# Kernel optimization log

Measured on AMD Instinct MI355X. Metric: run time of the kernel, lower is better.

Reference implementation:

```python
import jax, jax.numpy as jnp
import numpy as np

TEMPERATURE = 0.07
BASE_TEMPERATURE = 0.07


def _pairwise_euclid(x):
    # torch.cdist(x, x, p=2), with safe sqrt (zero grad at zero distance)
    sq = jnp.sum(x * x, axis=1)
    d2 = sq[:, None] + sq[None, :] - 2.0 * (x @ x.T)
    d2 = jnp.maximum(d2, 0.0)
    safe = jnp.where(d2 > 0.0, d2, 1.0)
    return jnp.where(d2 > 0.0, jnp.sqrt(safe), 0.0)


def setup_inputs() -> dict:
    key = jax.random.key(0)
    k1, k2 = jax.random.split(key)
    features = jax.random.normal(k1, (1024, 2, 512), dtype=jnp.float32)
    labels = jax.random.uniform(k2, (1024,), dtype=jnp.float32)
    return {"features": features, "labels": labels}


def reference(features, labels):
    B, V, D = features.shape
    N = B * V
    # torch.cat(torch.unbind(features, dim=1), dim=0): views stacked -> [N, D]
    cf = features.transpose(1, 0, 2).reshape(N, D)
    lab = jnp.tile(labels, V)  # label of row i is labels[i % B]

    dist = _pairwise_euclid(cf)              # [N, N]
    logits = -dist / TEMPERATURE
    eye = jnp.eye(N, dtype=logits.dtype)
    w = jnp.exp(logits) * (1.0 - eye)        # exp(logits) with l == i excluded

    dis = jnp.abs(lab[:, None] - lab[None, :])  # |y_i - y_j|, symmetric

    # negative[i, j] = sum_{l != i, |y_l - y_i| >= |y_i - y_j|} exp(logits[i, l])
    # computed per-row via sort + suffix cumsum + searchsorted (O(N^2 log N))
    order = jnp.argsort(dis, axis=1)
    sorted_d = jnp.take_along_axis(dis, order, axis=1)
    sorted_w = jnp.take_along_axis(w, order, axis=1)
    suffix = jnp.flip(jnp.cumsum(jnp.flip(sorted_w, axis=1), axis=1), axis=1)
    suffix = jnp.concatenate([suffix, jnp.zeros((N, 1), suffix.dtype)], axis=1)  # [N, N+1]
    # side='left': counts entries strictly < d, so suffix[idx] sums all >= d (ties incl.)
    idx = jax.vmap(lambda sd, d: jnp.searchsorted(sd, d, side='left'))(sorted_d, dis)
    negative = jnp.take_along_axis(suffix, idx, axis=1)
    negative = negative * (1.0 - eye) + eye  # diag set to 1 (log -> 0)

    logits_z = logits * (1.0 - eye)          # logits[i, i] = 0
    log_prob = logits_z - jnp.log(negative)
    mean_log_prob_pos = jnp.sum(log_prob, axis=1) / (N - 1)
    loss = -(TEMPERATURE / BASE_TEMPERATURE) * jnp.mean(mean_log_prob_pos)
    return loss
```

## Files before the change

kernel.cpp:

```cpp
#include <hip/hip_runtime.h>
#include <math.h>


#define NN 2048
#define BB 1024
#define DD 512
#define NT 256
#define NEGINF (-INFINITY)
#define CS 64.0f

typedef short s16x8 __attribute__((ext_vector_type(8)));
typedef float f32x4 __attribute__((ext_vector_type(4)));

__device__ __forceinline__ const float* cf_row(const float* F, int i) {
    return F + ((size_t)(i & (BB - 1)) * 2 + (size_t)(i >> 10)) * DD;
}

__device__ __forceinline__ unsigned bf_rne(float x) {
    const unsigned u = __float_as_uint(x);
    return (u + 0x7FFFu + ((u >> 16) & 1u)) >> 16;
}
__device__ __forceinline__ float bf_val(unsigned h) {
    return __uint_as_float(h << 16);
}

__global__ __launch_bounds__(512) void sort_labels_kernel(const float* __restrict__ labels,
                                                          float* __restrict__ slab,
                                                          int* __restrict__ sj) {
    __shared__ float kk[BB];
    __shared__ int   id[BB];
    const int t = threadIdx.x;
    #pragma unroll
    for (int e = 0; e < 2; ++e) { const int p = t + e * 512; kk[p] = labels[p]; id[p] = p; }
    for (int k = 2; k <= BB; k <<= 1) {
        for (int j = k >> 1; j > 0; j >>= 1) {
            if (j >= 32) __syncthreads();
            else __builtin_amdgcn_wave_barrier();
            #pragma unroll
            for (int e = 0; e < 2; ++e) {
                const int idx = t + e * 512;
                const int ixj = idx ^ j;
                if (ixj > idx) {
                    const float k1 = kk[idx], k2 = kk[ixj];
                    const bool up = ((idx & k) == 0);
                    if (up ? (k1 > k2) : (k1 < k2)) {
                        kk[idx] = k2; kk[ixj] = k1;
                        const int i1 = id[idx]; id[idx] = id[ixj]; id[ixj] = i1;
                    }
                }
            }
        }
    }
    __syncthreads();
    #pragma unroll
    for (int e = 0; e < 2; ++e) {
        const int p = t + e * 512;
        const float lv = kk[p];
        const int b = id[p];
        slab[2 * p] = lv; slab[2 * p + 1] = lv;
        sj[2 * p] = b;    sj[2 * p + 1] = b + BB;
    }
}

__global__ __launch_bounds__(256) void prep_split_kernel(const float* __restrict__ F,
                                                         ushort* __restrict__ Ahi,
                                                         ushort* __restrict__ Alo,
                                                         float* __restrict__ sq) {
    const int t = threadIdx.x;
    const int lane = t & 63;
    const int w = t >> 6;
    const int i = blockIdx.x * 4 + w;
    const float* src = cf_row(F, i);
    const float4 v0 = reinterpret_cast<const float4*>(src)[lane];
    const float4 v1 = reinterpret_cast<const float4*>(src)[lane + 64];
    float ss = v0.x * v0.x + v0.y * v0.y + v0.z * v0.z + v0.w * v0.w
             + v1.x * v1.x + v1.y * v1.y + v1.z * v1.z + v1.w * v1.w;
    #pragma unroll
    for (int st = 32; st > 0; st >>= 1) ss += __shfl_down(ss, st);
    if (lane == 0) sq[i] = ss;

    const float a[8] = {v0.x, v0.y, v0.z, v0.w, v1.x, v1.y, v1.z, v1.w};
    ushort h[8], l[8];
    #pragma unroll
    for (int e = 0; e < 8; ++e) {
        const unsigned hb = bf_rne(a[e]);
        h[e] = (ushort)hb;
        l[e] = (ushort)bf_rne(a[e] - bf_val(hb));
    }
    const size_t base = (size_t)i * DD;
    *reinterpret_cast<ushort4*>(&Ahi[base + lane * 4])       = make_ushort4(h[0], h[1], h[2], h[3]);
    *reinterpret_cast<ushort4*>(&Ahi[base + 256 + lane * 4]) = make_ushort4(h[4], h[5], h[6], h[7]);
    *reinterpret_cast<ushort4*>(&Alo[base + lane * 4])       = make_ushort4(l[0], l[1], l[2], l[3]);
    *reinterpret_cast<ushort4*>(&Alo[base + 256 + lane * 4]) = make_ushort4(l[4], l[5], l[6], l[7]);
}

#define TM 128
#define TN 64
#define TK 32
__global__ __launch_bounds__(256) void gemm_dist_kernel(const ushort* __restrict__ Ahi,
                                                        const ushort* __restrict__ Alo,
                                                        const float* __restrict__ sq,
                                                        const int* __restrict__ sj,
                                                        float* __restrict__ distp) {
    __shared__ ushort Ah[4][TM][8];
    __shared__ ushort Al[4][TM][8];
    __shared__ ushort Bh[4][TN][8];
    __shared__ ushort Bl[4][TN][8];
    __shared__ int   sjcA[TM];
    __shared__ int   sjcB[TN];
    __shared__ float sqA[TM];
    __shared__ float sqB[TN];

    const int t = threadIdx.x;
    const int lane = t & 63;
    const int w = t >> 6;

    const int id = blockIdx.x;
    int by = (int)((__fsqrt_rn(4.0f * (float)id + 1.0f) - 1.0f) * 0.5f);
    while ((by + 1) * (by + 2) <= id) ++by;
    while (by * (by + 1) > id) --by;
    const int bx = id - by * (by + 1);
    const int row0 = by * TM;
    const int col0 = bx * TN;
    const bool below = (bx < 2 * by);

    if (t < TM) {
        const int s = sj[row0 + t];
        sjcA[t] = s; sqA[t] = sq[s];
    } else if (t < TM + TN) {
        const int u = t - TM;
        const int s = sj[col0 + u];
        sjcB[u] = s; sqB[u] = sq[s];
    }
    __syncthreads();
    const int rr = t >> 2;
    const int cq = t & 3;
    const size_t gA0 = (size_t)sjcA[rr] * DD + cq * 8;
    const size_t gA1 = (size_t)sjcA[64 + rr] * DD + cq * 8;
    const size_t gB0 = (size_t)sjcB[rr] * DD + cq * 8;

    f32x4 acc[2][4] = {};
    const int m = lane & 15;
    const int q = lane >> 4;

    for (int kt = 0; kt < DD / TK; ++kt) {
        __syncthreads();
        const size_t ko = (size_t)kt * TK;
        *reinterpret_cast<int4*>(&Ah[cq][rr][0])      = *reinterpret_cast<const int4*>(&Ahi[gA0 + ko]);
        *reinterpret_cast<int4*>(&Al[cq][rr][0])      = *reinterpret_cast<const int4*>(&Alo[gA0 + ko]);
        *reinterpret_cast<int4*>(&Ah[cq][64 + rr][0]) = *reinterpret_cast<const int4*>(&Ahi[gA1 + ko]);
        *reinterpret_cast<int4*>(&Al[cq][64 + rr][0]) = *reinterpret_cast<const int4*>(&Alo[gA1 + ko]);
        *reinterpret_cast<int4*>(&Bh[cq][rr][0])      = *reinterpret_cast<const int4*>(&Ahi[gB0 + ko]);
        *reinterpret_cast<int4*>(&Bl[cq][rr][0])      = *reinterpret_cast<const int4*>(&Alo[gB0 + ko]);
        __syncthreads();

        s16x8 fah[2], fal[2], fbh[4], fbl[4];
        #pragma unroll
        for (int mt = 0; mt < 2; ++mt) {
            fah[mt] = *reinterpret_cast<const s16x8*>(&Ah[q][w * 32 + mt * 16 + m][0]);
            fal[mt] = *reinterpret_cast<const s16x8*>(&Al[q][w * 32 + mt * 16 + m][0]);
        }
        #pragma unroll
        for (int nt = 0; nt < 4; ++nt) {
            fbh[nt] = *reinterpret_cast<const s16x8*>(&Bh[q][nt * 16 + m][0]);
            fbl[nt] = *reinterpret_cast<const s16x8*>(&Bl[q][nt * 16 + m][0]);
        }
        #pragma unroll
        for (int mt = 0; mt < 2; ++mt)
            #pragma unroll
            for (int nt = 0; nt < 4; ++nt) {
                acc[mt][nt] = __builtin_amdgcn_mfma_f32_16x16x32_bf16(fah[mt], fbh[nt], acc[mt][nt], 0, 0, 0);
                acc[mt][nt] = __builtin_amdgcn_mfma_f32_16x16x32_bf16(fah[mt], fbl[nt], acc[mt][nt], 0, 0, 0);
                acc[mt][nt] = __builtin_amdgcn_mfma_f32_16x16x32_bf16(fal[mt], fbh[nt], acc[mt][nt], 0, 0, 0);
            }
    }

    #pragma unroll
    for (int mt = 0; mt < 2; ++mt) {
        const int lr0 = w * 32 + mt * 16 + q * 4;
        #pragma unroll
        for (int nt = 0; nt < 4; ++nt) {
            const int lc = nt * 16 + m;
            float o[4];
            #pragma unroll
            for (int r = 0; r < 4; ++r) {
                const float d2 = sqA[lr0 + r] + sqB[lc] - 2.0f * acc[mt][nt][r];
                o[r] = (d2 > 0.f) ? sqrtf(d2) : 0.f;
            }
            #pragma unroll
            for (int r = 0; r < 4; ++r)
                distp[(size_t)(row0 + lr0 + r) * NN + col0 + lc] = o[r];
            if (below) {
                const float4 o4 = make_float4(o[0], o[1], o[2], o[3]);
                *reinterpret_cast<float4*>(&distp[(size_t)(col0 + lc) * NN + row0 + lr0]) = o4;
            }
        }
    }
}

__device__ __forceinline__ int bs_right(const float* key, float d, int lo, int hi) {
    while (lo < hi) {
        const int mid = (lo + hi) >> 1;
        if (key[mid] >= d) hi = mid; else lo = mid + 1;
    }
    return lo;
}
__device__ __forceinline__ int bs_left(const float* key, float d, int lo, int hi) {
    while (lo < hi) {
        const int mid = (lo + hi) >> 1;
        if (key[mid] < d) hi = mid; else lo = mid + 1;
    }
    return lo;
}

__global__ __launch_bounds__(256) void row_kernel(const float* __restrict__ distp,
                                                  const float* __restrict__ slab,
                                                  double* __restrict__ rowval) {
    __shared__ float key[NN];
    __shared__ float Pf[NN];
    __shared__ float Sf[NN + 1];
    __shared__ float wmxA[4], wmxB[4], wps[4], wss[4];
    __shared__ double wDA[4], wLA[4], wDB[4], wLB[4];

    const int pr = blockIdx.x;
    const int rA = 2 * pr, rB = 2 * pr + 1;
    const int t = threadIdx.x;
    const int lane = t & 63;
    const int w = t >> 6;
    const float x = slab[rA];
    const float negInvT = -1.0f / 0.07f;
    const float* drowA = &distp[(size_t)rA * NN];
    const float* drowB = &distp[(size_t)rB * NN];

    #pragma unroll
    for (int e = 0; e < 2; ++e) {
        const int p4 = t + e * NT;
        const float4 l4 = reinterpret_cast<const float4*>(slab)[p4];
        key[p4 * 4 + 0] = fabsf(l4.x - x);
        key[p4 * 4 + 1] = fabsf(l4.y - x);
        key[p4 * 4 + 2] = fabsf(l4.z - x);
        key[p4 * 4 + 3] = fabsf(l4.w - x);
    }
    const int cb = t * 8;
    float vA[8], vB[8];
    double dsumA = 0.0, dsumB = 0.0;
    float mxA = NEGINF, mxB = NEGINF;
    #pragma unroll
    for (int e = 0; e < 2; ++e) {
        const float4 a4 = reinterpret_cast<const float4*>(drowA)[2 * t + e];
        const float4 b4 = reinterpret_cast<const float4*>(drowB)[2 * t + e];
        const float av[4] = {a4.x, a4.y, a4.z, a4.w};
        const float bv[4] = {b4.x, b4.y, b4.z, b4.w};
        #pragma unroll
        for (int c = 0; c < 4; ++c) {
            const int pc = cb + e * 4 + c;
            if (pc == rA) vA[e * 4 + c] = NEGINF;
            else { const float vv = av[c] * negInvT; vA[e * 4 + c] = vv; mxA = fmaxf(mxA, vv); dsumA += (double)av[c]; }
            if (pc == rB) vB[e * 4 + c] = NEGINF;
            else { const float vv = bv[c] * negInvT; vB[e * 4 + c] = vv; mxB = fmaxf(mxB, vv); dsumB += (double)bv[c]; }
        }
    }
    #pragma unroll
    for (int st = 32; st > 0; st >>= 1) {
        mxA = fmaxf(mxA, __shfl_down(mxA, st));
        mxB = fmaxf(mxB, __shfl_down(mxB, st));
    }
    if (lane == 0) { wmxA[w] = mxA; wmxB[w] = mxB; }
    __syncthreads();
    const float MA = fmaxf(fmaxf(wmxA[0], wmxA[1]), fmaxf(wmxA[2], wmxA[3]));
    const float MB = fmaxf(fmaxf(wmxB[0], wmxB[1]), fmaxf(wmxB[2], wmxB[3]));

    int L8[8], R8[8];
    const int a = cb, b = cb + 7;
    {
        const int le = (rA - 1 < b) ? rA - 1 : b;
        if (a <= le) {
            const float da = key[a];
            const int Ra = bs_right(key, da, rA, NN);
            int Rl = Ra;
            if (le > a) Rl = bs_right(key, key[le], rA, Ra);
            for (int p = a; p <= le; ++p) {
                const float d = key[p];
                int R;
                if (p == a) R = Ra;
                else if (p == le) R = Rl;
                else R = bs_right(key, d, Rl, Ra);
                int L = p + 1;
                while (L < rA && key[L] == d) ++L;
                L8[p - a] = L; R8[p - a] = R;
            }
        }
        const int rs = (rA + 1 > a) ? rA + 1 : a;
        if (rs <= b) {
            const float dr = key[rs];
            const int Lr = bs_left(key, dr, 0, rA);
            int Lb = Lr;
            if (b > rs) Lb = bs_left(key, key[b], 0, Lr);
            for (int p = rs; p <= b; ++p) {
                const float d = key[p];
                int L;
                if (p == rs) L = Lr;
                else if (p == b) L = Lb;
                else L = bs_left(key, d, Lb, Lr);
                int R = p;
                while (R > rA && key[R - 1] == d) --R;
                L8[p - a] = L; R8[p - a] = R;
            }
        }
        if (rA >= a && rA <= b) { L8[rA - a] = rA; R8[rA - a] = rA; }
    }

    double lnsumA = 0.0;
    {
        float e8[8];
        #pragma unroll
        for (int jj = 0; jj < 8; ++jj) e8[jj] = __expf(vA[jj] - MA + CS);
        {
            float run = 0.f, ex[8];
            #pragma unroll
            for (int jj = 0; jj < 8; ++jj) { ex[jj] = run; run += e8[jj]; }
            float inc = run;
            #pragma unroll
            for (int st = 1; st < 64; st <<= 1) {
                const float nm = __shfl_up(inc, st);
                if (lane >= st) inc += nm;
            }
            float xofs = __shfl_up(inc, 1);
            if (lane == 0) xofs = 0.f;
            if (lane == 63) wps[w] = inc;
            __syncthreads();
            #pragma unroll
            for (int ww = 0; ww < 3; ++ww)
                if (ww < w) xofs += wps[ww];
            #pragma unroll
            for (int jj = 0; jj < 8; ++jj) Pf[cb + jj] = ex[jj] + xofs;
        }
        {
            float run = 0.f, sx[8];
            #pragma unroll
            for (int jj = 7; jj >= 0; --jj) { run += e8[jj]; sx[jj] = run; }
            float inc = run;
            #pragma unroll
            for (int st = 1; st < 64; st <<= 1) {
                const float nm = __shfl_down(inc, st);
                if (lane + st < 64) inc += nm;
            }
            float xofs = __shfl_down(inc, 1);
            if (lane == 63) xofs = 0.f;
            if (lane == 0) wss[w] = inc;
            __syncthreads();
            #pragma unroll
            for (int ww = 1; ww < 4; ++ww)
                if (ww > w) xofs += wss[ww];
            #pragma unroll
            for (int jj = 0; jj < 8; ++jj) Sf[cb + jj] = sx[jj] + xofs;
            if (t == 0) Sf[NN] = 0.f;
        }
        __syncthreads();
        const float MBA = MA - CS;
        #pragma unroll
        for (int jj = 0; jj < 8; ++jj) {
            const int p = cb + jj;
            if (p == rA) continue;
            const float s = fmaxf(Pf[L8[jj]] + Sf[R8[jj]], 1e-38f);
            lnsumA += (double)(MBA + __logf(s));
        }
    }
    __syncthreads();

    double lnsumB = 0.0;
    {
        float e8[8];
        #pragma unroll
        for (int jj = 0; jj < 8; ++jj) e8[jj] = __expf(vB[jj] - MB + CS);
        {
            float run = 0.f, ex[8];
            #pragma unroll
            for (int jj = 0; jj < 8; ++jj) { ex[jj] = run; run += e8[jj]; }
            float inc = run;
            #pragma unroll
            for (int st = 1; st < 64; st <<= 1) {
                const float nm = __shfl_up(inc, st);
                if (lane >= st) inc += nm;
            }
            float xofs = __shfl_up(inc, 1);
            if (lane == 0) xofs = 0.f;
            if (lane == 63) wps[w] = inc;
            __syncthreads();
            #pragma unroll
            for (int ww = 0; ww < 3; ++ww)
                if (ww < w) xofs += wps[ww];
            #pragma unroll
            for (int jj = 0; jj < 8; ++jj) Pf[cb + jj] = ex[jj] + xofs;
        }
        {
            float run = 0.f, sx[8];
            #pragma unroll
            for (int jj = 7; jj >= 0; --jj) { run += e8[jj]; sx[jj] = run; }
            float inc = run;
            #pragma unroll
            for (int st = 1; st < 64; st <<= 1) {
                const float nm = __shfl_down(inc, st);
                if (lane + st < 64) inc += nm;
            }
            float xofs = __shfl_down(inc, 1);
            if (lane == 63) xofs = 0.f;
            if (lane == 0) wss[w] = inc;
            __syncthreads();
            #pragma unroll
            for (int ww = 1; ww < 4; ++ww)
                if (ww > w) xofs += wss[ww];
            #pragma unroll
            for (int jj = 0; jj < 8; ++jj) Sf[cb + jj] = sx[jj] + xofs;
            if (t == 0) Sf[NN] = 0.f;
        }
        __syncthreads();
        const float MBB = MB - CS;
        #pragma unroll
        for (int jj = 0; jj < 8; ++jj) {
            const int p = cb + jj;
            if (p == rB) continue;
            const float s = fmaxf(Pf[L8[jj]] + Sf[R8[jj]], 1e-38f);
            lnsumB += (double)(MBB + __logf(s));
        }
    }

    #pragma unroll
    for (int st = 32; st > 0; st >>= 1) {
        dsumA  += __shfl_down(dsumA, st);
        lnsumA += __shfl_down(lnsumA, st);
        dsumB  += __shfl_down(dsumB, st);
        lnsumB += __shfl_down(lnsumB, st);
    }
    if (lane == 0) { wDA[w] = dsumA; wLA[w] = lnsumA; wDB[w] = dsumB; wLB[w] = lnsumB; }
    __syncthreads();
    if (t == 0) {
        rowval[rA] = (-(wDA[0] + wDA[1] + wDA[2] + wDA[3]) / 0.07)
                   - (wLA[0] + wLA[1] + wLA[2] + wLA[3]);
        rowval[rB] = (-(wDB[0] + wDB[1] + wDB[2] + wDB[3]) / 0.07)
                   - (wLB[0] + wLB[1] + wLB[2] + wLB[3]);
    }
}

__global__ __launch_bounds__(256) void finalize_kernel(const double* __restrict__ rowval,
                                                       float* __restrict__ out) {
    __shared__ double red[NT];
    const int t = threadIdx.x;
    double s = 0.0;
    for (int j = t; j < NN; j += NT) s += rowval[j];
    red[t] = s;
    __syncthreads();
    for (int ofs = NT / 2; ofs > 0; ofs >>= 1) {
        if (t < ofs) red[t] += red[t + ofs];
        __syncthreads();
    }
    if (t == 0) {
        out[0] = (float)(-red[0] / ((double)NN * (double)(NN - 1)));
    }
}

extern "C" void kernel_launch(void* const* d_in, const int* in_sizes, int n_in,
                              void* d_out, int out_size, void* d_ws, size_t ws_size,
                              hipStream_t stream) {
    const float* features = (const float*)d_in[0];
    const float* labels   = (const float*)d_in[1];
    float* out = (float*)d_out;

    char* ws = (char*)d_ws;
    size_t off = 0;
    float*  sq     = (float*) (ws + off); off += NN * sizeof(float);
    float*  slab   = (float*) (ws + off); off += NN * sizeof(float);
    int*    sj     = (int*)   (ws + off); off += NN * sizeof(int);
    double* rowval = (double*)(ws + off); off += NN * sizeof(double);
    ushort* Ahi    = (ushort*)(ws + off); off += (size_t)NN * DD * sizeof(ushort);
    ushort* Alo    = (ushort*)(ws + off); off += (size_t)NN * DD * sizeof(ushort);
    float*  distp  = (float*) (ws + off); off += (size_t)NN * NN * sizeof(float);

    sort_labels_kernel<<<1, 512, 0, stream>>>(labels, slab, sj);
    prep_split_kernel<<<NN / 4, NT, 0, stream>>>(features, Ahi, Alo, sq);
    gemm_dist_kernel<<<16 * 17, NT, 0, stream>>>(Ahi, Alo, sq, sj, distp);
    row_kernel<<<NN / 2, NT, 0, stream>>>(distp, slab, rowval);
    finalize_kernel<<<1, NT, 0, stream>>>(rowval, out);
}
```

Baseline: 133.1 us.

## Fuse label ranking sort into prep kernel, shrink GEMM tiles, widen row blocks

Replaces the single-block bitonic label sort with a parallel rank-counting sort placed in extra blocks of the feature split/prep kernel, removing one launch and the serial sort latency. Halves the GEMM row tile to 64 so the triangular grid has more blocks to fill the GPU, at the cost of less operand reuse per block. Row kernel uses 512 threads with 4 elements per thread for more parallelism per row pair.

```diff
diff --git a/kernel.cpp b/kernel.cpp
--- a/kernel.cpp
+++ b/kernel.cpp
@@ -24,77 +24,68 @@
     return __uint_as_float(h << 16);
 }
 
-__global__ __launch_bounds__(512) void sort_labels_kernel(const float* __restrict__ labels,
-                                                          float* __restrict__ slab,
-                                                          int* __restrict__ sj) {
-    __shared__ float kk[BB];
-    __shared__ int   id[BB];
+__global__ __launch_bounds__(512) void prep_sort_kernel(const float* __restrict__ F,
+                                                        const float* __restrict__ labels,
+                                                        ushort* __restrict__ Ahi,
+                                                        ushort* __restrict__ Alo,
+                                                        float* __restrict__ sq,
+                                                        float* __restrict__ slab,
+                                                        int* __restrict__ sj) {
+    __shared__ float lab[BB];
+    const int blk = blockIdx.x;
     const int t = threadIdx.x;
-    #pragma unroll
-    for (int e = 0; e < 2; ++e) { const int p = t + e * 512; kk[p] = labels[p]; id[p] = p; }
-    for (int k = 2; k <= BB; k <<= 1) {
-        for (int j = k >> 1; j > 0; j >>= 1) {
-            if (j >= 32) __syncthreads();
-            else __builtin_amdgcn_wave_barrier();
-            #pragma unroll
-            for (int e = 0; e < 2; ++e) {
-                const int idx = t + e * 512;
-                const int ixj = idx ^ j;
-                if (ixj > idx) {
-                    const float k1 = kk[idx], k2 = kk[ixj];
-                    const bool up = ((idx & k) == 0);
-                    if (up ? (k1 > k2) : (k1 < k2)) {
-                        kk[idx] = k2; kk[ixj] = k1;
-                        const int i1 = id[idx]; id[idx] = id[ixj]; id[ixj] = i1;
-                    }
-                }
-            }
-        }
-    }
-    __syncthreads();
-    #pragma unroll
-    for (int e = 0; e < 2; ++e) {
-        const int p = t + e * 512;
-        const float lv = kk[p];
-        const int b = id[p];
-        slab[2 * p] = lv; slab[2 * p + 1] = lv;
-        sj[2 * p] = b;    sj[2 * p + 1] = b + BB;
-    }
-}
-
-__global__ __launch_bounds__(256) void prep_split_kernel(const float* __restrict__ F,
-                                                         ushort* __restrict__ Ahi,
-                                                         ushort* __restrict__ Alo,
-                                                         float* __restrict__ sq) {
-    const int t = threadIdx.x;
-    const int lane = t & 63;
-    const int w = t >> 6;
-    const int i = blockIdx.x * 4 + w;
-    const float* src = cf_row(F, i);
-    const float4 v0 = reinterpret_cast<const float4*>(src)[lane];
-    const float4 v1 = reinterpret_cast<const float4*>(src)[lane + 64];
-    float ss = v0.x * v0.x + v0.y * v0.y + v0.z * v0.z + v0.w * v0.w
-             + v1.x * v1.x + v1.y * v1.y + v1.z * v1.z + v1.w * v1.w;
-    #pragma unroll
-    for (int st = 32; st > 0; st >>= 1) ss += __shfl_down(ss, st);
-    if (lane == 0) sq[i] = ss;
-
-    const float a[8] = {v0.x, v0.y, v0.z, v0.w, v1.x, v1.y, v1.z, v1.w};
-    ushort h[8], l[8];
-    #pragma unroll
-    for (int e = 0; e < 8; ++e) {
-        const unsigned hb = bf_rne(a[e]);
-        h[e] = (ushort)hb;
-        l[e] = (ushort)bf_rne(a[e] - bf_val(hb));
-    }
-    const size_t base = (size_t)i * DD;
-    *reinterpret_cast<ushort4*>(&Ahi[base + lane * 4])       = make_ushort4(h[0], h[1], h[2], h[3]);
-    *reinterpret_cast<ushort4*>(&Ahi[base + 256 + lane * 4]) = make_ushort4(h[4], h[5], h[6], h[7]);
-    *reinterpret_cast<ushort4*>(&Alo[base + lane * 4])       = make_ushort4(l[0], l[1], l[2], l[3]);
-    *reinterpret_cast<ushort4*>(&Alo[base + 256 + lane * 4]) = make_ushort4(l[4], l[5], l[6], l[7]);
-}
-
-#define TM 128
+
+    if (blk < 256) {
+        const int lane = t & 63;
+        const int w = t >> 6;
+        const int i = blk * 8 + w;
+        const float* src = cf_row(F, i);
+        const float4 v0 = reinterpret_cast<const float4*>(src)[lane];
+        const float4 v1 = reinterpret_cast<const float4*>(src)[lane + 64];
+        float ss = v0.x * v0.x + v0.y * v0.y + v0.z * v0.z + v0.w * v0.w
+                 + v1.x * v1.x + v1.y * v1.y + v1.z * v1.z + v1.w * v1.w;
+        #pragma unroll
+        for (int st = 32; st > 0; st >>= 1) ss += __shfl_down(ss, st);
+        if (lane == 0) sq[i] = ss;
+
+        const float a[8] = {v0.x, v0.y, v0.z, v0.w, v1.x, v1.y, v1.z, v1.w};
+        ushort h[8], l[8];
+        #pragma unroll
+        for (int e = 0; e < 8; ++e) {
+            const unsigned hb = bf_rne(a[e]);
+            h[e] = (ushort)hb;
+            l[e] = (ushort)bf_rne(a[e] - bf_val(hb));
+        }
+        const size_t base = (size_t)i * DD;
+        *reinterpret_cast<ushort4*>(&Ahi[base + lane * 4])       = make_ushort4(h[0], h[1], h[2], h[3]);
+        *reinterpret_cast<ushort4*>(&Ahi[base + 256 + lane * 4]) = make_ushort4(h[4], h[5], h[6], h[7]);
+        *reinterpret_cast<ushort4*>(&Alo[base + lane * 4])       = make_ushort4(l[0], l[1], l[2], l[3]);
+        *reinterpret_cast<ushort4*>(&Alo[base + 256 + lane * 4]) = make_ushort4(l[4], l[5], l[6], l[7]);
+    } else {
+        lab[t] = labels[t];
+        lab[t + 512] = labels[t + 512];
+        __syncthreads();
+        const int e = (blk - 256) * 512 + t;
+        const float li = lab[e];
+        int rank = 0;
+        const float4* l4 = reinterpret_cast<const float4*>(lab);
+        #pragma unroll 4
+        for (int j = 0; j < BB / 4; ++j) {
+            const float4 v = l4[j];
+            const int j0 = j * 4;
+            rank += (v.x < li) || (v.x == li && (j0 + 0) < e);
+            rank += (v.y < li) || (v.y == li && (j0 + 1) < e);
+            rank += (v.z < li) || (v.z == li && (j0 + 2) < e);
+            rank += (v.w < li) || (v.w == li && (j0 + 3) < e);
+        }
+        slab[2 * rank]     = li;
+        slab[2 * rank + 1] = li;
+        sj[2 * rank]     = e;
+        sj[2 * rank + 1] = e + BB;
+    }
+}
+
+#define TM 64
 #define TN 64
 #define TK 32
 __global__ __launch_bounds__(256) void gemm_dist_kernel(const ushort* __restrict__ Ahi,
@@ -116,13 +107,13 @@
     const int w = t >> 6;
 
     const int id = blockIdx.x;
-    int by = (int)((__fsqrt_rn(4.0f * (float)id + 1.0f) - 1.0f) * 0.5f);
-    while ((by + 1) * (by + 2) <= id) ++by;
-    while (by * (by + 1) > id) --by;
-    const int bx = id - by * (by + 1);
+    int by = (int)((__fsqrt_rn(8.0f * (float)id + 1.0f) - 1.0f) * 0.5f);
+    while ((by + 1) * (by + 2) / 2 <= id) ++by;
+    while (by * (by + 1) / 2 > id) --by;
+    const int bx = id - by * (by + 1) / 2;
     const int row0 = by * TM;
     const int col0 = bx * TN;
-    const bool below = (bx < 2 * by);
+    const bool below = (bx < by);
 
     if (t < TM) {
         const int s = sj[row0 + t];
@@ -135,65 +126,50 @@
     __syncthreads();
     const int rr = t >> 2;
     const int cq = t & 3;
-    const size_t gA0 = (size_t)sjcA[rr] * DD + cq * 8;
-    const size_t gA1 = (size_t)sjcA[64 + rr] * DD + cq * 8;
-    const size_t gB0 = (size_t)sjcB[rr] * DD + cq * 8;
-
-    f32x4 acc[2][4] = {};
+    const size_t gA = (size_t)sjcA[rr] * DD + cq * 8;
+    const size_t gB = (size_t)sjcB[rr] * DD + cq * 8;
+
+    f32x4 acc[4] = {};
     const int m = lane & 15;
     const int q = lane >> 4;
 
     for (int kt = 0; kt < DD / TK; ++kt) {
         __syncthreads();
         const size_t ko = (size_t)kt * TK;
-        *reinterpret_cast<int4*>(&Ah[cq][rr][0])      = *reinterpret_cast<const int4*>(&Ahi[gA0 + ko]);
-        *reinterpret_cast<int4*>(&Al[cq][rr][0])      = *reinterpret_cast<const int4*>(&Alo[gA0 + ko]);
-        *reinterpret_cast<int4*>(&Ah[cq][64 + rr][0]) = *reinterpret_cast<const int4*>(&Ahi[gA1 + ko]);
-        *reinterpret_cast<int4*>(&Al[cq][64 + rr][0]) = *reinterpret_cast<const int4*>(&Alo[gA1 + ko]);
-        *reinterpret_cast<int4*>(&Bh[cq][rr][0])      = *reinterpret_cast<const int4*>(&Ahi[gB0 + ko]);
-        *reinterpret_cast<int4*>(&Bl[cq][rr][0])      = *reinterpret_cast<const int4*>(&Alo[gB0 + ko]);
-        __syncthreads();
-
-        s16x8 fah[2], fal[2], fbh[4], fbl[4];
-        #pragma unroll
-        for (int mt = 0; mt < 2; ++mt) {
-            fah[mt] = *reinterpret_cast<const s16x8*>(&Ah[q][w * 32 + mt * 16 + m][0]);
-            fal[mt] = *reinterpret_cast<const s16x8*>(&Al[q][w * 32 + mt * 16 + m][0]);
-        }
+        *reinterpret_cast<int4*>(&Ah[cq][rr][0]) = *reinterpret_cast<const int4*>(&Ahi[gA + ko]);
+        *reinterpret_cast<int4*>(&Al[cq][rr][0]) = *reinterpret_cast<const int4*>(&Alo[gA + ko]);
+        *reinterpret_cast<int4*>(&Bh[cq][rr][0]) = *reinterpret_cast<const int4*>(&Ahi[gB + ko]);
+        *reinterpret_cast<int4*>(&Bl[cq][rr][0]) = *reinterpret_cast<const int4*>(&Alo[gB + ko]);
+        __syncthreads();
+
+        const s16x8 fah = *reinterpret_cast<const s16x8*>(&Ah[q][w * 16 + m][0]);
+        const s16x8 fal = *reinterpret_cast<const s16x8*>(&Al[q][w * 16 + m][0]);
         #pragma unroll
         for (int nt = 0; nt < 4; ++nt) {
-            fbh[nt] = *reinterpret_cast<const s16x8*>(&Bh[q][nt * 16 + m][0]);
-            fbl[nt] = *reinterpret_cast<const s16x8*>(&Bl[q][nt * 16 + m][0]);
-        }
-        #pragma unroll
-        for (int mt = 0; mt < 2; ++mt)
-            #pragma unroll
-            for (int nt = 0; nt < 4; ++nt) {
-                acc[mt][nt] = __builtin_amdgcn_mfma_f32_16x16x32_bf16(fah[mt], fbh[nt], acc[mt][nt], 0, 0, 0);
-                acc[mt][nt] = __builtin_amdgcn_mfma_f32_16x16x32_bf16(fah[mt], fbl[nt], acc[mt][nt], 0, 0, 0);
-                acc[mt][nt] = __builtin_amdgcn_mfma_f32_16x16x32_bf16(fal[mt], fbh[nt], acc[mt][nt], 0, 0, 0);
-            }
-    }
-
+            const s16x8 fbh = *reinterpret_cast<const s16x8*>(&Bh[q][nt * 16 + m][0]);
+            const s16x8 fbl = *reinterpret_cast<const s16x8*>(&Bl[q][nt * 16 + m][0]);
+            acc[nt] = __builtin_amdgcn_mfma_f32_16x16x32_bf16(fah, fbh, acc[nt], 0, 0, 0);
+            acc[nt] = __builtin_amdgcn_mfma_f32_16x16x32_bf16(fah, fbl, acc[nt], 0, 0, 0);
+            acc[nt] = __builtin_amdgcn_mfma_f32_16x16x32_bf16(fal, fbh, acc[nt], 0, 0, 0);
+        }
+    }
+
+    const int lr0 = w * 16 + q * 4;
     #pragma unroll
-    for (int mt = 0; mt < 2; ++mt) {
-        const int lr0 = w * 32 + mt * 16 + q * 4;
-        #pragma unroll
-        for (int nt = 0; nt < 4; ++nt) {
-            const int lc = nt * 16 + m;
-            float o[4];
-            #pragma unroll
-            for (int r = 0; r < 4; ++r) {
-                const float d2 = sqA[lr0 + r] + sqB[lc] - 2.0f * acc[mt][nt][r];
-                o[r] = (d2 > 0.f) ? sqrtf(d2) : 0.f;
-            }
-            #pragma unroll
-            for (int r = 0; r < 4; ++r)
-                distp[(size_t)(row0 + lr0 + r) * NN + col0 + lc] = o[r];
-            if (below) {
-                const float4 o4 = make_float4(o[0], o[1], o[2], o[3]);
-                *reinterpret_cast<float4*>(&distp[(size_t)(col0 + lc) * NN + row0 + lr0]) = o4;
-            }
+    for (int nt = 0; nt < 4; ++nt) {
+        const int lc = nt * 16 + m;
+        float o[4];
+        #pragma unroll
+        for (int r = 0; r < 4; ++r) {
+            const float d2 = sqA[lr0 + r] + sqB[lc] - 2.0f * acc[nt][r];
+            o[r] = (d2 > 0.f) ? sqrtf(d2) : 0.f;
+        }
+        #pragma unroll
+        for (int r = 0; r < 4; ++r)
+            distp[(size_t)(row0 + lr0 + r) * NN + col0 + lc] = o[r];
+        if (below) {
+            const float4 o4 = make_float4(o[0], o[1], o[2], o[3]);
+            *reinterpret_cast<float4*>(&distp[(size_t)(col0 + lc) * NN + row0 + lr0]) = o4;
         }
     }
 }
@@ -213,14 +189,14 @@
     return lo;
 }
 
-__global__ __launch_bounds__(256) void row_kernel(const float* __restrict__ distp,
+__global__ __launch_bounds__(512) void row_kernel(const float* __restrict__ distp,
                                                   const float* __restrict__ slab,
                                                   double* __restrict__ rowval) {
     __shared__ float key[NN];
     __shared__ float Pf[NN];
     __shared__ float Sf[NN + 1];
-    __shared__ float wmxA[4], wmxB[4], wps[4], wss[4];
-    __shared__ double wDA[4], wLA[4], wDB[4], wLB[4];
+    __shared__ float wmxA[8], wmxB[8], wps[8], wss[8];
+    __shared__ double wDA[8], wLA[8], wDB[8], wLB[8];
 
     const int pr = blockIdx.x;
     const int rA = 2 * pr, rB = 2 * pr + 1;
@@ -232,32 +208,29 @@
     const float* drowA = &distp[(size_t)rA * NN];
     const float* drowB = &distp[(size_t)rB * NN];
 
-    #pragma unroll
-    for (int e = 0; e < 2; ++e) {
-        const int p4 = t + e * NT;
-        const float4 l4 = reinterpret_cast<const float4*>(slab)[p4];
-        key[p4 * 4 + 0] = fabsf(l4.x - x);
-        key[p4 * 4 + 1] = fabsf(l4.y - x);
-        key[p4 * 4 + 2] = fabsf(l4.z - x);
-        key[p4 * 4 + 3] = fabsf(l4.w - x);
-    }
-    const int cb = t * 8;
-    float vA[8], vB[8];
+    {
+        const float4 l4 = reinterpret_cast<const float4*>(slab)[t];
+        key[t * 4 + 0] = fabsf(l4.x - x);
+        key[t * 4 + 1] = fabsf(l4.y - x);
+        key[t * 4 + 2] = fabsf(l4.z - x);
+        key[t * 4 + 3] = fabsf(l4.w - x);
+    }
+    const int cb = t * 4;
+    float vA[4], vB[4];
     double dsumA = 0.0, dsumB = 0.0;
     float mxA = NEGINF, mxB = NEGINF;
-    #pragma unroll
-    for (int e = 0; e < 2; ++e) {
-        const float4 a4 = reinterpret_cast<const float4*>(drowA)[2 * t + e];
-        const float4 b4 = reinterpret_cast<const float4*>(drowB)[2 * t + e];
+    {
+        const float4 a4 = reinterpret_cast<const float4*>(drowA)[t];
+        const float4 b4 = reinterpret_cast<const float4*>(drowB)[t];
         const float av[4] = {a4.x, a4.y, a4.z, a4.w};
         const float bv[4] = {b4.x, b4.y, b4.z, b4.w};
         #pragma unroll
         for (int c = 0; c < 4; ++c) {
-            const int pc = cb + e * 4 + c;
-            if (pc == rA) vA[e * 4 + c] = NEGINF;
-            else { const float vv = av[c] * negInvT; vA[e * 4 + c] = vv; mxA = fmaxf(mxA, vv); dsumA += (double)av[c]; }
-            if (pc == rB) vB[e * 4 + c] = NEGINF;
-            else { const float vv = bv[c] * negInvT; vB[e * 4 + c] = vv; mxB = fmaxf(mxB, vv); dsumB += (double)bv[c]; }
+            const int pc = cb + c;
+            if (pc == rA) vA[c] = NEGINF;
+            else { const float vv = av[c] * negInvT; vA[c] = vv; mxA = fmaxf(mxA, vv); dsumA += (double)av[c]; }
+            if (pc == rB) vB[c] = NEGINF;
+            else { const float vv = bv[c] * negInvT; vB[c] = vv; mxB = fmaxf(mxB, vv); dsumB += (double)bv[c]; }
         }
     }
     #pragma unroll
@@ -267,11 +240,13 @@
     }
     if (lane == 0) { wmxA[w] = mxA; wmxB[w] = mxB; }
     __syncthreads();
-    const float MA = fmaxf(fmaxf(wmxA[0], wmxA[1]), fmaxf(wmxA[2], wmxA[3]));
-    const float MB = fmaxf(fmaxf(wmxB[0], wmxB[1]), fmaxf(wmxB[2], wmxB[3]));
-
-    int L8[8], R8[8];
-    const int a = cb, b = cb + 7;
+    const float MA = fmaxf(fmaxf(fmaxf(wmxA[0], wmxA[1]), fmaxf(wmxA[2], wmxA[3])),
+                           fmaxf(fmaxf(wmxA[4], wmxA[5]), fmaxf(wmxA[6], wmxA[7])));
+    const float MB = fmaxf(fmaxf(fmaxf(wmxB[0], wmxB[1]), fmaxf(wmxB[2], wmxB[3])),
+                           fmaxf(fmaxf(wmxB[4], wmxB[5]), fmaxf(wmxB[6], wmxB[7])));
+
+    int L8[4], R8[4];
+    const int a = cb, b = cb + 3;
     {
         const int le = (rA - 1 < b) ? rA - 1 : b;
         if (a <= le) {
@@ -312,13 +287,13 @@
 
     double lnsumA = 0.0;
     {
-        float e8[8];
-        #pragma unroll
-        for (int jj = 0; jj < 8; ++jj) e8[jj] = __expf(vA[jj] - MA + CS);
+        float e8[4];
+        #pragma unroll
+        for (int jj = 0; jj < 4; ++jj) e8[jj] = __expf(vA[jj] - MA + CS);
         {
-            float run = 0.f, ex[8];
-            #pragma unroll
-            for (int jj = 0; jj < 8; ++jj) { ex[jj] = run; run += e8[jj]; }
+            float run = 0.f, ex[4];
+            #pragma unroll
+            for (int jj = 0; jj < 4; ++jj) { ex[jj] = run; run += e8[jj]; }
             float inc = run;
             #pragma unroll
             for (int st = 1; st < 64; st <<= 1) {
@@ -330,15 +305,15 @@
             if (lane == 63) wps[w] = inc;
             __syncthreads();
             #pragma unroll
-            for (int ww = 0; ww < 3; ++ww)
+            for (int ww = 0; ww < 7; ++ww)
                 if (ww < w) xofs += wps[ww];
             #pragma unroll
-            for (int jj = 0; jj < 8; ++jj) Pf[cb + jj] = ex[jj] + xofs;
+            for (int jj = 0; jj < 4; ++jj) Pf[cb + jj] = ex[jj] + xofs;
         }
         {
-            float run = 0.f, sx[8];
-            #pragma unroll
-            for (int jj = 7; jj >= 0; --jj) { run += e8[jj]; sx[jj] = run; }
+            float run = 0.f, sx[4];
+            #pragma unroll
+            for (int jj = 3; jj >= 0; --jj) { run += e8[jj]; sx[jj] = run; }
             float inc = run;
             #pragma unroll
             for (int st = 1; st < 64; st <<= 1) {
@@ -350,16 +325,16 @@
             if (lane == 0) wss[w] = inc;
             __syncthreads();
             #pragma unroll
-            for (int ww = 1; ww < 4; ++ww)
+            for (int ww = 1; ww < 8; ++ww)
                 if (ww > w) xofs += wss[ww];
             #pragma unroll
-            for (int jj = 0; jj < 8; ++jj) Sf[cb + jj] = sx[jj] + xofs;
+            for (int jj = 0; jj < 4; ++jj) Sf[cb + jj] = sx[jj] + xofs;
             if (t == 0) Sf[NN] = 0.f;
         }
         __syncthreads();
         const float MBA = MA - CS;
         #pragma unroll
-        for (int jj = 0; jj < 8; ++jj) {
+        for (int jj = 0; jj < 4; ++jj) {
             const int p = cb + jj;
             if (p == rA) continue;
             const float s = fmaxf(Pf[L8[jj]] + Sf[R8[jj]], 1e-38f);
@@ -370,13 +345,13 @@
 
     double lnsumB = 0.0;
     {
-        float e8[8];
-        #pragma unroll
-        for (int jj = 0; jj < 8; ++jj) e8[jj] = __expf(vB[jj] - MB + CS);
+        float e8[4];
+        #pragma unroll
+        for (int jj = 0; jj < 4; ++jj) e8[jj] = __expf(vB[jj] - MB + CS);
         {
-            float run = 0.f, ex[8];
-            #pragma unroll
-            for (int jj = 0; jj < 8; ++jj) { ex[jj] = run; run += e8[jj]; }
+            float run = 0.f, ex[4];
+            #pragma unroll
+            for (int jj = 0; jj < 4; ++jj) { ex[jj] = run; run += e8[jj]; }
             float inc = run;
             #pragma unroll
             for (int st = 1; st < 64; st <<= 1) {
@@ -388,15 +363,15 @@
             if (lane == 63) wps[w] = inc;
             __syncthreads();
             #pragma unroll
-            for (int ww = 0; ww < 3; ++ww)
+            for (int ww = 0; ww < 7; ++ww)
                 if (ww < w) xofs += wps[ww];
             #pragma unroll
-            for (int jj = 0; jj < 8; ++jj) Pf[cb + jj] = ex[jj] + xofs;
+            for (int jj = 0; jj < 4; ++jj) Pf[cb + jj] = ex[jj] + xofs;
         }
         {
-            float run = 0.f, sx[8];
-            #pragma unroll
-            for (int jj = 7; jj >= 0; --jj) { run += e8[jj]; sx[jj] = run; }
+            float run = 0.f, sx[4];
+            #pragma unroll
+            for (int jj = 3; jj >= 0; --jj) { run += e8[jj]; sx[jj] = run; }
             float inc = run;
             #pragma unroll
             for (int st = 1; st < 64; st <<= 1) {
@@ -408,16 +383,16 @@
             if (lane == 0) wss[w] = inc;
             __syncthreads();
             #pragma unroll
-            for (int ww = 1; ww < 4; ++ww)
+            for (int ww = 1; ww < 8; ++ww)
                 if (ww > w) xofs += wss[ww];
             #pragma unroll
-            for (int jj = 0; jj < 8; ++jj) Sf[cb + jj] = sx[jj] + xofs;
+            for (int jj = 0; jj < 4; ++jj) Sf[cb + jj] = sx[jj] + xofs;
             if (t == 0) Sf[NN] = 0.f;
         }
         __syncthreads();
         const float MBB = MB - CS;
         #pragma unroll
-        for (int jj = 0; jj < 8; ++jj) {
+        for (int jj = 0; jj < 4; ++jj) {
             const int p = cb + jj;
             if (p == rB) continue;
             const float s = fmaxf(Pf[L8[jj]] + Sf[R8[jj]], 1e-38f);
@@ -435,10 +410,11 @@
     if (lane == 0) { wDA[w] = dsumA; wLA[w] = lnsumA; wDB[w] = dsumB; wLB[w] = lnsumB; }
     __syncthreads();
     if (t == 0) {
-        rowval[rA] = (-(wDA[0] + wDA[1] + wDA[2] + wDA[3]) / 0.07)
-                   - (wLA[0] + wLA[1] + wLA[2] + wLA[3]);
-        rowval[rB] = (-(wDB[0] + wDB[1] + wDB[2] + wDB[3]) / 0.07)
-                   - (wLB[0] + wLB[1] + wLB[2] + wLB[3]);
+        double dA = 0.0, lA = 0.0, dB = 0.0, lB = 0.0;
+        #pragma unroll
+        for (int ww = 0; ww < 8; ++ww) { dA += wDA[ww]; lA += wLA[ww]; dB += wDB[ww]; lB += wLB[ww]; }
+        rowval[rA] = (-dA / 0.07) - lA;
+        rowval[rB] = (-dB / 0.07) - lB;
     }
 }
 
@@ -476,9 +452,8 @@
     ushort* Alo    = (ushort*)(ws + off); off += (size_t)NN * DD * sizeof(ushort);
     float*  distp  = (float*) (ws + off); off += (size_t)NN * NN * sizeof(float);
 
-    sort_labels_kernel<<<1, 512, 0, stream>>>(labels, slab, sj);
-    prep_split_kernel<<<NN / 4, NT, 0, stream>>>(features, Ahi, Alo, sq);
-    gemm_dist_kernel<<<16 * 17, NT, 0, stream>>>(Ahi, Alo, sq, sj, distp);
-    row_kernel<<<NN / 2, NT, 0, stream>>>(distp, slab, rowval);
+    prep_sort_kernel<<<258, 512, 0, stream>>>(features, labels, Ahi, Alo, sq, slab, sj);
+    gemm_dist_kernel<<<528, NT, 0, stream>>>(Ahi, Alo, sq, sj, distp);
+    row_kernel<<<NN / 2, 512, 0, stream>>>(distp, slab, rowval);
     finalize_kernel<<<1, NT, 0, stream>>>(rowval, out);
 }
```

Measured after the change: 136.7 us. 2.7% more time.

## Fuse label sort into prep kernel via rank sort; fold finalize into row kernel

Applied to the files above, without the earlier changes.

Replaces the single-block bitonic label sort with a parallel rank-counting sort, run as two extra blocks inside the feature split/prep kernel, so the sort and the bf16 split happen in one launch. The separate finalize kernel is removed: each row-pair block atomically adds its double contribution, and the last block (found with an atomic counter) writes the loss. This cuts two kernel launches and the serial bitonic stage. The cost is global atomics and a summation order that is no longer deterministic. The rank sort does O(N) compares per element.

```diff
diff --git a/kernel.cpp b/kernel.cpp
--- a/kernel.cpp
+++ b/kernel.cpp
@@ -24,74 +24,68 @@
     return __uint_as_float(h << 16);
 }
 
-__global__ __launch_bounds__(512) void sort_labels_kernel(const float* __restrict__ labels,
-                                                          float* __restrict__ slab,
-                                                          int* __restrict__ sj) {
-    __shared__ float kk[BB];
-    __shared__ int   id[BB];
+__global__ __launch_bounds__(512) void prep_sort_kernel(const float* __restrict__ F,
+                                                        const float* __restrict__ labels,
+                                                        ushort* __restrict__ Ahi,
+                                                        ushort* __restrict__ Alo,
+                                                        float* __restrict__ sq,
+                                                        float* __restrict__ slab,
+                                                        int* __restrict__ sj,
+                                                        double* __restrict__ accd,
+                                                        int* __restrict__ cnt) {
+    __shared__ float lab[BB];
+    const int blk = blockIdx.x;
     const int t = threadIdx.x;
-    #pragma unroll
-    for (int e = 0; e < 2; ++e) { const int p = t + e * 512; kk[p] = labels[p]; id[p] = p; }
-    for (int k = 2; k <= BB; k <<= 1) {
-        for (int j = k >> 1; j > 0; j >>= 1) {
-            if (j >= 32) __syncthreads();
-            else __builtin_amdgcn_wave_barrier();
-            #pragma unroll
-            for (int e = 0; e < 2; ++e) {
-                const int idx = t + e * 512;
-                const int ixj = idx ^ j;
-                if (ixj > idx) {
-                    const float k1 = kk[idx], k2 = kk[ixj];
-                    const bool up = ((idx & k) == 0);
-                    if (up ? (k1 > k2) : (k1 < k2)) {
-                        kk[idx] = k2; kk[ixj] = k1;
-                        const int i1 = id[idx]; id[idx] = id[ixj]; id[ixj] = i1;
-                    }
-                }
-            }
-        }
-    }
-    __syncthreads();
-    #pragma unroll
-    for (int e = 0; e < 2; ++e) {
-        const int p = t + e * 512;
-        const float lv = kk[p];
-        const int b = id[p];
-        slab[2 * p] = lv; slab[2 * p + 1] = lv;
-        sj[2 * p] = b;    sj[2 * p + 1] = b + BB;
-    }
-}
-
-__global__ __launch_bounds__(256) void prep_split_kernel(const float* __restrict__ F,
-                                                         ushort* __restrict__ Ahi,
-                                                         ushort* __restrict__ Alo,
-                                                         float* __restrict__ sq) {
-    const int t = threadIdx.x;
-    const int lane = t & 63;
-    const int w = t >> 6;
-    const int i = blockIdx.x * 4 + w;
-    const float* src = cf_row(F, i);
-    const float4 v0 = reinterpret_cast<const float4*>(src)[lane];
-    const float4 v1 = reinterpret_cast<const float4*>(src)[lane + 64];
-    float ss = v0.x * v0.x + v0.y * v0.y + v0.z * v0.z + v0.w * v0.w
-             + v1.x * v1.x + v1.y * v1.y + v1.z * v1.z + v1.w * v1.w;
-    #pragma unroll
-    for (int st = 32; st > 0; st >>= 1) ss += __shfl_down(ss, st);
-    if (lane == 0) sq[i] = ss;
-
-    const float a[8] = {v0.x, v0.y, v0.z, v0.w, v1.x, v1.y, v1.z, v1.w};
-    ushort h[8], l[8];
-    #pragma unroll
-    for (int e = 0; e < 8; ++e) {
-        const unsigned hb = bf_rne(a[e]);
-        h[e] = (ushort)hb;
-        l[e] = (ushort)bf_rne(a[e] - bf_val(hb));
-    }
-    const size_t base = (size_t)i * DD;
-    *reinterpret_cast<ushort4*>(&Ahi[base + lane * 4])       = make_ushort4(h[0], h[1], h[2], h[3]);
-    *reinterpret_cast<ushort4*>(&Ahi[base + 256 + lane * 4]) = make_ushort4(h[4], h[5], h[6], h[7]);
-    *reinterpret_cast<ushort4*>(&Alo[base + lane * 4])       = make_ushort4(l[0], l[1], l[2], l[3]);
-    *reinterpret_cast<ushort4*>(&Alo[base + 256 + lane * 4]) = make_ushort4(l[4], l[5], l[6], l[7]);
+
+    if (blk < 256) {
+        const int lane = t & 63;
+        const int w = t >> 6;
+        const int i = blk * 8 + w;
+        const float* src = cf_row(F, i);
+        const float4 v0 = reinterpret_cast<const float4*>(src)[lane];
+        const float4 v1 = reinterpret_cast<const float4*>(src)[lane + 64];
+        float ss = v0.x * v0.x + v0.y * v0.y + v0.z * v0.z + v0.w * v0.w
+                 + v1.x * v1.x + v1.y * v1.y + v1.z * v1.z + v1.w * v1.w;
+        #pragma unroll
+        for (int st = 32; st > 0; st >>= 1) ss += __shfl_down(ss, st);
+        if (lane == 0) sq[i] = ss;
+
+        const float a[8] = {v0.x, v0.y, v0.z, v0.w, v1.x, v1.y, v1.z, v1.w};
+        ushort h[8], l[8];
+        #pragma unroll
+        for (int e = 0; e < 8; ++e) {
+            const unsigned hb = bf_rne(a[e]);
+            h[e] = (ushort)hb;
+            l[e] = (ushort)bf_rne(a[e] - bf_val(hb));
+        }
+        const size_t base = (size_t)i * DD;
+        *reinterpret_cast<ushort4*>(&Ahi[base + lane * 4])       = make_ushort4(h[0], h[1], h[2], h[3]);
+        *reinterpret_cast<ushort4*>(&Ahi[base + 256 + lane * 4]) = make_ushort4(h[4], h[5], h[6], h[7]);
+        *reinterpret_cast<ushort4*>(&Alo[base + lane * 4])       = make_ushort4(l[0], l[1], l[2], l[3]);
+        *reinterpret_cast<ushort4*>(&Alo[base + 256 + lane * 4]) = make_ushort4(l[4], l[5], l[6], l[7]);
+    } else {
+        if (blk == 257 && t == 0) { *accd = 0.0; *cnt = 0; }
+        lab[t] = labels[t];
+        lab[t + 512] = labels[t + 512];
+        __syncthreads();
+        const int e = (blk - 256) * 512 + t;
+        const float li = lab[e];
+        int rank = 0;
+        const float4* l4 = reinterpret_cast<const float4*>(lab);
+        #pragma unroll 4
+        for (int j = 0; j < BB / 4; ++j) {
+            const float4 v = l4[j];
+            const int j0 = j * 4;
+            rank += (v.x < li) || (v.x == li && (j0 + 0) < e);
+            rank += (v.y < li) || (v.y == li && (j0 + 1) < e);
+            rank += (v.z < li) || (v.z == li && (j0 + 2) < e);
+            rank += (v.w < li) || (v.w == li && (j0 + 3) < e);
+        }
+        slab[2 * rank]     = li;
+        slab[2 * rank + 1] = li;
+        sj[2 * rank]     = e;
+        sj[2 * rank + 1] = e + BB;
+    }
 }
 
 #define TM 128
@@ -215,7 +209,9 @@
 
 __global__ __launch_bounds__(256) void row_kernel(const float* __restrict__ distp,
                                                   const float* __restrict__ slab,
-                                                  double* __restrict__ rowval) {
+                                                  double* __restrict__ accd,
+                                                  int* __restrict__ cnt,
+                                                  float* __restrict__ out) {
     __shared__ float key[NN];
     __shared__ float Pf[NN];
     __shared__ float Sf[NN + 1];
@@ -435,27 +431,18 @@
     if (lane == 0) { wDA[w] = dsumA; wLA[w] = lnsumA; wDB[w] = dsumB; wLB[w] = lnsumB; }
     __syncthreads();
     if (t == 0) {
-        rowval[rA] = (-(wDA[0] + wDA[1] + wDA[2] + wDA[3]) / 0.07)
-                   - (wLA[0] + wLA[1] + wLA[2] + wLA[3]);
-        rowval[rB] = (-(wDB[0] + wDB[1] + wDB[2] + wDB[3]) / 0.07)
-                   - (wLB[0] + wLB[1] + wLB[2] + wLB[3]);
-    }
-}
-
-__global__ __launch_bounds__(256) void finalize_kernel(const double* __restrict__ rowval,
-                                                       float* __restrict__ out) {
-    __shared__ double red[NT];
-    const int t = threadIdx.x;
-    double s = 0.0;
-    for (int j = t; j < NN; j += NT) s += rowval[j];
-    red[t] = s;
-    __syncthreads();
-    for (int ofs = NT / 2; ofs > 0; ofs >>= 1) {
-        if (t < ofs) red[t] += red[t + ofs];
-        __syncthreads();
-    }
-    if (t == 0) {
-        out[0] = (float)(-red[0] / ((double)NN * (double)(NN - 1)));
+        const double pairv = ((-(wDA[0] + wDA[1] + wDA[2] + wDA[3]) / 0.07)
+                              - (wLA[0] + wLA[1] + wLA[2] + wLA[3]))
+                           + ((-(wDB[0] + wDB[1] + wDB[2] + wDB[3]) / 0.07)
+                              - (wLB[0] + wLB[1] + wLB[2] + wLB[3]));
+        atomicAdd(accd, pairv);
+        __threadfence();
+        const int old = atomicAdd(cnt, 1);
+        if (old == NN / 2 - 1) {
+            __threadfence();
+            const double tot = atomicAdd(accd, 0.0);
+            out[0] = (float)(-tot / ((double)NN * (double)(NN - 1)));
+        }
     }
 }
 
@@ -471,14 +458,13 @@
     float*  sq     = (float*) (ws + off); off += NN * sizeof(float);
     float*  slab   = (float*) (ws + off); off += NN * sizeof(float);
     int*    sj     = (int*)   (ws + off); off += NN * sizeof(int);
-    double* rowval = (double*)(ws + off); off += NN * sizeof(double);
+    double* accd   = (double*)(ws + off); off += sizeof(double);
+    int*    cnt    = (int*)   (ws + off); off += 2 * sizeof(int);
     ushort* Ahi    = (ushort*)(ws + off); off += (size_t)NN * DD * sizeof(ushort);
     ushort* Alo    = (ushort*)(ws + off); off += (size_t)NN * DD * sizeof(ushort);
     float*  distp  = (float*) (ws + off); off += (size_t)NN * NN * sizeof(float);
 
-    sort_labels_kernel<<<1, 512, 0, stream>>>(labels, slab, sj);
-    prep_split_kernel<<<NN / 4, NT, 0, stream>>>(features, Ahi, Alo, sq);
+    prep_sort_kernel<<<258, 512, 0, stream>>>(features, labels, Ahi, Alo, sq, slab, sj, accd, cnt);
     gemm_dist_kernel<<<16 * 17, NT, 0, stream>>>(Ahi, Alo, sq, sj, distp);
-    row_kernel<<<NN / 2, NT, 0, stream>>>(distp, slab, rowval);
-    finalize_kernel<<<1, NT, 0, stream>>>(rowval, out);
-}
+    row_kernel<<<NN / 2, NT, 0, stream>>>(distp, slab, accd, cnt, out);
+}
```

New measurement: 160.9 us. 1.21x slower.
